# Kernel tuning notes

Hardware: AMD Instinct MI355X
Metric: run time of the kernel (lower is better)

Reference implementation:

```python
import jax, jax.numpy as jnp
import numpy as np

B, C, H, W = 32, 512, 32, 32
CI = C // 2  # inter_channels
EPS = 1e-5


def setup_inputs() -> dict:
    key = jax.random.key(0)
    ks = jax.random.split(key, 12)
    s = 0.02
    return {
        "x": jax.random.normal(ks[0], (B, C, H, W), jnp.float32),
        "w_g": jax.random.normal(ks[1], (CI, C), jnp.float32) * s,
        "b_g": jax.random.normal(ks[2], (CI,), jnp.float32) * s,
        "w_theta": jax.random.normal(ks[3], (CI, C), jnp.float32) * s,
        "b_theta": jax.random.normal(ks[4], (CI,), jnp.float32) * s,
        "w_phi": jax.random.normal(ks[5], (CI, C), jnp.float32) * s,
        "b_phi": jax.random.normal(ks[6], (CI,), jnp.float32) * s,
        "w_W": jax.random.normal(ks[7], (C, CI), jnp.float32) * s,
        "b_W": jax.random.normal(ks[8], (C,), jnp.float32) * s,
        "bn_gamma": jax.random.normal(ks[9], (C,), jnp.float32) * 0.1 + 1.0,
        "bn_beta": jax.random.normal(ks[10], (C,), jnp.float32) * 0.1,
        "bn_mean": jax.random.normal(ks[11], (C,), jnp.float32) * 0.1,
        "bn_var": jnp.abs(jax.random.normal(jax.random.fold_in(key, 99), (C,), jnp.float32)) * 0.5 + 0.5,
    }


def reference(x, w_g, b_g, w_theta, b_theta, w_phi, b_phi, w_W, b_W,
              bn_gamma, bn_beta, bn_mean, bn_var):
    b, c, h, w = x.shape
    n = h * w
    xf = x.reshape(b, c, n)  # [B, C, N]
    # 1x1 convs == per-pixel channel matmuls
    g = jnp.einsum('oc,bcn->bon', w_g, xf) + b_g[:, None]          # [B, Ci, N]
    theta = jnp.einsum('oc,bcn->bon', w_theta, xf) + b_theta[:, None]
    phi = jnp.einsum('oc,bcn->bon', w_phi, xf) + b_phi[:, None]
    # f[b, i, j] = theta_i . phi_j ; scaled by 1/N (softmax-free attention)
    f_div_C = jnp.einsum('bcn,bcm->bnm', theta, phi) / n           # [B, N, N]
    # y[b, c, n] = sum_m f[b, n, m] * g[b, c, m]
    y = jnp.einsum('bnm,bcm->bcn', f_div_C, g)                     # [B, Ci, N]
    # W: 1x1 conv back to C channels + BatchNorm (inference form)
    Wy = jnp.einsum('oi,bin->bon', w_W, y) + b_W[:, None]          # [B, C, N]
    inv_std = jax.lax.rsqrt(bn_var + EPS)
    bn = (Wy - bn_mean[:, None]) * (inv_std * bn_gamma)[:, None] + bn_beta[:, None]
    z = bn.reshape(b, c, h, w) + x
    return z
```

## Files before the change

kernel.cpp:

```cpp
#include <hip/hip_runtime.h>
#include <hip/hip_bf16.h>
#include <cstdint>
#include <cstddef>

using bf16 = __hip_bfloat16;
typedef __attribute__((ext_vector_type(8))) short short8v;
typedef __attribute__((ext_vector_type(4))) float f32x4;

static constexpr int BATCH = 32;
static constexpr int CH    = 512;
static constexpr int CIc   = 256;
static constexpr int NSP   = 1024;
#define EPSV 1e-5f

__device__ __forceinline__ bf16 f2bf(float f) { return __float2bfloat16(f); }

__device__ __forceinline__ void gload_lds16(const bf16* g, bf16* l) {
  __builtin_amdgcn_global_load_lds(
      (const __attribute__((address_space(1))) void*)g,
      (__attribute__((address_space(3))) void*)l, 16, 0, 0);
}

__global__ __launch_bounds__(256) void convert_weights(
    const float* __restrict__ wg, const float* __restrict__ wph, const float* __restrict__ wth,
    const float* __restrict__ bg, const float* __restrict__ bph, const float* __restrict__ bth,
    const float* __restrict__ wW,
    bf16* __restrict__ wcat, bf16* __restrict__ wWb, float* __restrict__ biascat)
{
  int i = blockIdx.x * 256 + threadIdx.x;
  const int WSZ = CIc * CH;
  if (i < WSZ) {
    wcat[i]         = f2bf(wg[i]);
    wcat[WSZ + i]   = f2bf(wph[i]);
    wcat[2*WSZ + i] = f2bf(wth[i]);
    wWb[i]          = f2bf(wW[i]);
  }
  if (i < CIc) {
    biascat[i]        = bg[i];
    biascat[CIc + i]  = bph[i];
    biascat[2*CIc + i]= bth[i];
  }
}

__global__ __launch_bounds__(256) void transpose_x_kernel(
    const float* __restrict__ x, bf16* __restrict__ xt)
{
  __shared__ bf16 t[32][34];
  int n0 = blockIdx.x * 32, c0 = blockIdx.y * 32, b = blockIdx.z;
  const float* s = x + (size_t)b * CH * NSP;
  bf16* d = xt + (size_t)b * NSP * CH;
  int tx = threadIdx.x & 31, ty = threadIdx.x >> 5;
  #pragma unroll
  for (int i = 0; i < 32; i += 8)
    t[ty + i][tx] = f2bf(s[(size_t)(c0 + ty + i) * NSP + n0 + tx]);
  __syncthreads();
  #pragma unroll
  for (int i = 0; i < 32; i += 8)
    d[(size_t)(n0 + ty + i) * CH + c0 + tx] = t[tx][ty + i];
}

template<int EPI>
__global__ __launch_bounds__(512, 4) void gemm_bt(
    const bf16* __restrict__ A, size_t sA,
    const bf16* __restrict__ Bm, size_t sB,
    void* __restrict__ Cm,
    int K,
    const float* __restrict__ bias,
    bf16* __restrict__ Tt,
    const float* __restrict__ bW, const float* __restrict__ gma,
    const float* __restrict__ bta, const float* __restrict__ mu,
    const float* __restrict__ var,
    const float* __restrict__ xres)
{
  __shared__ bf16 As[2][256 * 32];
  __shared__ bf16 Bs[2][128 * 32];
  int m0, n0, zb;
  if constexpr (EPI == 1) {
    int bidx = blockIdx.x;
    int wg = (bidx & 7) * 96 + (bidx >> 3);
    m0 = (wg >> 8) * 256;
    n0 = (wg & 255) * 128;
    zb = 0;
  } else {
    m0 = blockIdx.y * 256; n0 = blockIdx.x * 128; zb = blockIdx.z;
  }
  const bf16* Ab = A  + (size_t)zb * sA;
  const bf16* Bb = Bm + (size_t)zb * sB;
  const int tid  = threadIdx.x;
  const int wv   = tid >> 6, lane = tid & 63;
  const int l16  = lane & 15, g4 = lane >> 4;
  const int wr   = wv >> 1,  wc = wv & 1;

  f32x4 acc[4][4];
  #pragma unroll
  for (int i = 0; i < 4; ++i)
    #pragma unroll
    for (int j = 0; j < 4; ++j)
      acc[i][j] = (f32x4){0.f, 0.f, 0.f, 0.f};

  const int rq  = lane >> 2;
  const int oct = (lane & 3) ^ ((lane >> 3) & 3);
  auto stage = [&](int t, int p) {
    int kb = t * 32 + oct * 8;
    #pragma unroll
    for (int i = 0; i < 2; ++i) {
      int f = wv * 2 + i;
      gload_lds16(Ab + (size_t)(m0 + f * 16 + rq) * K + kb, &As[p][f * 512]);
    }
    gload_lds16(Bb + (size_t)(n0 + wv * 16 + rq) * K + kb, &Bs[p][wv * 512]);
  };

  const int rs = (g4 ^ ((l16 >> 1) & 3)) * 8;
  const int nt = K >> 5;
  stage(0, 0);
  __syncthreads();
  for (int t = 0; t < nt; ++t) {
    const int cur = t & 1;
    if (t + 1 < nt) stage(t + 1, cur ^ 1);
    short8v af[4], bfv[4];
    #pragma unroll
    for (int mf = 0; mf < 4; ++mf)
      af[mf] = *(const short8v*)&As[cur][(wr * 64 + mf * 16 + l16) * 32 + rs];
    #pragma unroll
    for (int nf = 0; nf < 4; ++nf)
      bfv[nf] = *(const short8v*)&Bs[cur][(wc * 64 + nf * 16 + l16) * 32 + rs];
    #pragma unroll
    for (int mf = 0; mf < 4; ++mf)
      #pragma unroll
      for (int nf = 0; nf < 4; ++nf)
        acc[mf][nf] = __builtin_amdgcn_mfma_f32_16x16x32_bf16(af[mf], bfv[nf], acc[mf][nf], 0, 0, 0);
    __syncthreads();
  }

  const int colbase = n0 + wc * 64 + l16;
  const int rowb    = wr * 64 + g4 * 4;

  if constexpr (EPI == 2) {
    #pragma unroll
    for (int mf = 0; mf < 4; ++mf) {
      #pragma unroll
      for (int j = 0; j < 4; ++j) {
        int row = m0 + rowb + mf * 16 + j;
        float a  = gma[row] * rsqrtf(var[row] + EPSV);
        float bb = (bW[row] - mu[row]) * a + bta[row];
        float sc = a * (1.f / (float)NSP);
        #pragma unroll
        for (int nf = 0; nf < 4; ++nf) {
          int col = colbase + nf * 16;
          size_t idx = (size_t)zb * (CH * NSP) + (size_t)row * NSP + col;
          ((float*)Cm)[idx] = acc[mf][nf][j] * sc + bb + ((const float*)xres)[idx];
        }
      }
    }
  } else {
    if (m0 < 512) {
      #pragma unroll
      for (int mf = 0; mf < 4; ++mf)
        #pragma unroll
        for (int j = 0; j < 4; ++j) {
          int row = m0 + rowb + mf * 16 + j;
          float badd = bias[row];
          #pragma unroll
          for (int nf = 0; nf < 4; ++nf) {
            int col = colbase + nf * 16;
            int b = col >> 10, n = col & 1023;
            ((bf16*)Cm)[(size_t)b * (CH * NSP) + (size_t)row * NSP + n] = f2bf(acc[mf][nf][j] + badd);
          }
        }
    } else {
      #pragma unroll
      for (int mf = 0; mf < 4; ++mf) {
        int ci0 = rowb + mf * 16;
        #pragma unroll
        for (int nf = 0; nf < 4; ++nf) {
          int col = colbase + nf * 16;
          int b = col >> 10, n = col & 1023;
          uint64_t pk = 0;
          #pragma unroll
          for (int j = 0; j < 4; ++j) {
            bf16 bv = f2bf(acc[mf][nf][j] + bias[512 + ci0 + j]);
            pk |= (uint64_t)(*(unsigned short*)&bv) << (16 * j);
          }
          *(uint64_t*)(Tt + (size_t)b * (NSP * CIc) + (size_t)n * CIc + ci0) = pk;
        }
      }
    }
  }
}

__global__ __launch_bounds__(256) void gemm_nt_small(
    const bf16* __restrict__ A, size_t sA,
    const bf16* __restrict__ Bm, size_t sB,
    bf16* __restrict__ Cm, size_t sC,
    int N, int K)
{
  __shared__ bf16 As[2][128 * 64];
  __shared__ bf16 Bs[2][128 * 64];
  const int b  = blockIdx.z;
  const int m0 = blockIdx.y * 128;
  const int n0 = blockIdx.x * 128;
  const bf16* Ab = A  + (size_t)b * sA;
  const bf16* Bb = Bm + (size_t)b * sB;
  const int tid  = threadIdx.x;
  const int wv   = tid >> 6, lane = tid & 63;
  const int l16  = lane & 15, g4 = lane >> 4;
  const int wr   = wv >> 1,  wc = wv & 1;

  f32x4 acc[4][4];
  #pragma unroll
  for (int i = 0; i < 4; ++i)
    #pragma unroll
    for (int j = 0; j < 4; ++j)
      acc[i][j] = (f32x4){0.f, 0.f, 0.f, 0.f};

  auto stage = [&](int ks, int p) {
    #pragma unroll
    for (int i = 0; i < 4; ++i) {
      int s = i * 256 + tid;
      int row = s >> 3, ch8 = (s & 7) << 3;
      gload_lds16(Ab + (size_t)(m0 + row) * K + ks + ch8, &As[p][(i * 256 + wv * 64) * 8]);
      gload_lds16(Bb + (size_t)(n0 + row) * K + ks + ch8, &Bs[p][(i * 256 + wv * 64) * 8]);
    }
  };

  const int nt = K >> 6;
  stage(0, 0);
  __syncthreads();
  for (int t = 0; t < nt; ++t) {
    const int cur = t & 1;
    if (t + 1 < nt) stage((t + 1) << 6, cur ^ 1);
    #pragma unroll
    for (int kk = 0; kk < 2; ++kk) {
      short8v af[4], bfv[4];
      #pragma unroll
      for (int mf = 0; mf < 4; ++mf)
        af[mf] = *(const short8v*)&As[cur][(wr * 64 + mf * 16 + l16) * 64 + kk * 32 + g4 * 8];
      #pragma unroll
      for (int nf = 0; nf < 4; ++nf)
        bfv[nf] = *(const short8v*)&Bs[cur][(wc * 64 + nf * 16 + l16) * 64 + kk * 32 + g4 * 8];
      #pragma unroll
      for (int mf = 0; mf < 4; ++mf)
        #pragma unroll
        for (int nf = 0; nf < 4; ++nf)
          acc[mf][nf] = __builtin_amdgcn_mfma_f32_16x16x32_bf16(af[mf], bfv[nf], acc[mf][nf], 0, 0, 0);
    }
    __syncthreads();
  }

  const int colbase = n0 + wc * 64 + l16;
  const int rowbase = m0 + wr * 64 + g4 * 4;
  #pragma unroll
  for (int mf = 0; mf < 4; ++mf)
    #pragma unroll
    for (int j = 0; j < 4; ++j) {
      int row = rowbase + mf * 16 + j;
      #pragma unroll
      for (int nf = 0; nf < 4; ++nf) {
        int col = colbase + nf * 16;
        Cm[(size_t)b * sC + (size_t)row * N + col] = f2bf(acc[mf][nf][j]);
      }
    }
}

extern "C" void kernel_launch(void* const* d_in, const int* in_sizes, int n_in,
                              void* d_out, int out_size, void* d_ws, size_t ws_size,
                              hipStream_t stream)
{
  const float* x    = (const float*)d_in[0];
  const float* w_g  = (const float*)d_in[1];
  const float* b_g  = (const float*)d_in[2];
  const float* w_th = (const float*)d_in[3];
  const float* b_th = (const float*)d_in[4];
  const float* w_ph = (const float*)d_in[5];
  const float* b_ph = (const float*)d_in[6];
  const float* w_W  = (const float*)d_in[7];
  const float* b_W  = (const float*)d_in[8];
  const float* gma  = (const float*)d_in[9];
  const float* bta  = (const float*)d_in[10];
  const float* mu   = (const float*)d_in[11];
  const float* var  = (const float*)d_in[12];
  float* out = (float*)d_out;

  char* ws = (char*)d_ws;
  bf16* proj = (bf16*)(ws + 0);
  bf16* xt   = (bf16*)(ws + 33554432);
  bf16* thT  = (bf16*)(ws + 67108864);
  bf16* S    = (bf16*)(ws + 83886080);
  bf16* T    = (bf16*)(ws + 88080384);
  bf16* wcat = (bf16*)(ws + 96468992);
  bf16* wWb  = (bf16*)(ws + 97255424);
  float* bcat= (float*)(ws + 97517568);

  convert_weights<<<512, 256, 0, stream>>>(w_g, w_ph, w_th, b_g, b_ph, b_th, w_W, wcat, wWb, bcat);
  transpose_x_kernel<<<dim3(32, 16, 32), 256, 0, stream>>>(x, xt);

  gemm_bt<1><<<dim3(768, 1, 1), 512, 0, stream>>>(
      wcat, 0, xt, 0, proj, CH, bcat, thT,
      nullptr, nullptr, nullptr, nullptr, nullptr, nullptr);

  gemm_nt_small<<<dim3(2, 2, 32), 256, 0, stream>>>(
      proj + 256 * 1024, (size_t)CH * NSP, proj, (size_t)CH * NSP, S, (size_t)CIc * CIc,
      CIc, NSP);

  gemm_nt_small<<<dim3(2, 4, 32), 256, 0, stream>>>(
      wWb, 0, S, (size_t)CIc * CIc, T, (size_t)CH * CIc,
      CIc, CIc);

  gemm_bt<2><<<dim3(8, 2, 32), 512, 0, stream>>>(
      T, (size_t)CH * CIc, thT, (size_t)NSP * CIc, out, CIc,
      nullptr, nullptr, b_W, gma, bta, mu, var, x);
}
```

Before: 132.1 us.

## Fuse x transpose and bf16 conversion into projection GEMM B-tile loading

Removes the separate transpose kernel and the xt bf16 workspace. The projection GEMM now reads fp32 x directly from global memory in its native [C,N] layout, converts each value to bf16 in registers, and writes swizzled B tiles into LDS, with the next tile's loads overlapped with the MFMA loop. This saves one kernel launch and a full write plus re-read of the transposed copy of x. In exchange, B loads become strided scalar fp32 reads issued through registers rather than direct global-to-LDS loads, which may lower load efficiency.

Measured after the change: 133.8 us. About the same (+1.3%).

```diff
diff --git a/kernel.cpp b/kernel.cpp
--- a/kernel.cpp
+++ b/kernel.cpp
@@ -42,31 +42,130 @@
   }
 }
 
-__global__ __launch_bounds__(256) void transpose_x_kernel(
-    const float* __restrict__ x, bf16* __restrict__ xt)
-{
-  __shared__ bf16 t[32][34];
-  int n0 = blockIdx.x * 32, c0 = blockIdx.y * 32, b = blockIdx.z;
-  const float* s = x + (size_t)b * CH * NSP;
-  bf16* d = xt + (size_t)b * NSP * CH;
-  int tx = threadIdx.x & 31, ty = threadIdx.x >> 5;
-  #pragma unroll
-  for (int i = 0; i < 32; i += 8)
-    t[ty + i][tx] = f2bf(s[(size_t)(c0 + ty + i) * NSP + n0 + tx]);
+__global__ __launch_bounds__(512, 4) void gemm_k1_fused(
+    const bf16* __restrict__ A,
+    const float* __restrict__ x,
+    bf16* __restrict__ Cm,
+    const float* __restrict__ bias,
+    bf16* __restrict__ Tt)
+{
+  constexpr int K = CH;
+  __shared__ bf16 As[2][256 * 32];
+  __shared__ bf16 Bs[2][128 * 32];
+  int bidx = blockIdx.x;
+  int wg = (bidx & 7) * 96 + (bidx >> 3);
+  const int m0 = (wg >> 8) * 256;
+  const int ncol = (wg & 255);
+  const int zb = ncol >> 3;
+  const int n0 = (ncol & 7) * 128;
+  const float* xb = x + (size_t)zb * (CH * NSP);
+  const int tid  = threadIdx.x;
+  const int wv   = tid >> 6, lane = tid & 63;
+  const int l16  = lane & 15, g4 = lane >> 4;
+  const int wr   = wv >> 1,  wc = wv & 1;
+
+  f32x4 acc[4][4];
+  #pragma unroll
+  for (int i = 0; i < 4; ++i)
+    #pragma unroll
+    for (int j = 0; j < 4; ++j)
+      acc[i][j] = (f32x4){0.f, 0.f, 0.f, 0.f};
+
+  const int rq  = lane >> 2;
+  const int aoct = (lane & 3) ^ ((lane >> 3) & 3);
+  auto stageA = [&](int t, int p) {
+    int kb = t * 32 + aoct * 8;
+    #pragma unroll
+    for (int i = 0; i < 2; ++i) {
+      int f = wv * 2 + i;
+      gload_lds16(A + (size_t)(m0 + f * 16 + rq) * K + kb, &As[p][f * 512]);
+    }
+  };
+
+  const int colq = tid >> 2;
+  const int octq = tid & 3;
+  const int bslot = octq ^ ((colq >> 1) & 3);
+  float vb[8];
+  auto loadB = [&](int t) {
+    const float* xp = xb + (size_t)(t * 32 + octq * 8) * NSP + n0 + colq;
+    #pragma unroll
+    for (int i = 0; i < 8; ++i) vb[i] = xp[(size_t)i * NSP];
+  };
+  auto writeB = [&](int p) {
+    short8v pk;
+    #pragma unroll
+    for (int i = 0; i < 8; ++i) {
+      bf16 bv = f2bf(vb[i]);
+      pk[i] = *(short*)&bv;
+    }
+    *(short8v*)&Bs[p][colq * 32 + bslot * 8] = pk;
+  };
+
+  const int rs = (g4 ^ ((l16 >> 1) & 3)) * 8;
+  const int nt = K >> 5;
+  loadB(0); stageA(0, 0); writeB(0);
   __syncthreads();
-  #pragma unroll
-  for (int i = 0; i < 32; i += 8)
-    d[(size_t)(n0 + ty + i) * CH + c0 + tx] = t[tx][ty + i];
-}
-
-template<int EPI>
-__global__ __launch_bounds__(512, 4) void gemm_bt(
+  for (int t = 0; t < nt; ++t) {
+    const int cur = t & 1;
+    if (t + 1 < nt) { stageA(t + 1, cur ^ 1); loadB(t + 1); }
+    short8v af[4], bfv[4];
+    #pragma unroll
+    for (int mf = 0; mf < 4; ++mf)
+      af[mf] = *(const short8v*)&As[cur][(wr * 64 + mf * 16 + l16) * 32 + rs];
+    #pragma unroll
+    for (int nf = 0; nf < 4; ++nf)
+      bfv[nf] = *(const short8v*)&Bs[cur][(wc * 64 + nf * 16 + l16) * 32 + rs];
+    #pragma unroll
+    for (int mf = 0; mf < 4; ++mf)
+      #pragma unroll
+      for (int nf = 0; nf < 4; ++nf)
+        acc[mf][nf] = __builtin_amdgcn_mfma_f32_16x16x32_bf16(af[mf], bfv[nf], acc[mf][nf], 0, 0, 0);
+    if (t + 1 < nt) writeB(cur ^ 1);
+    __syncthreads();
+  }
+
+  const int colbase = n0 + (zb << 10) + wc * 64 + l16;
+  const int rowb    = wr * 64 + g4 * 4;
+
+  if (m0 < 512) {
+    #pragma unroll
+    for (int mf = 0; mf < 4; ++mf)
+      #pragma unroll
+      for (int j = 0; j < 4; ++j) {
+        int row = m0 + rowb + mf * 16 + j;
+        float badd = bias[row];
+        #pragma unroll
+        for (int nf = 0; nf < 4; ++nf) {
+          int col = colbase + nf * 16;
+          int b = col >> 10, n = col & 1023;
+          Cm[(size_t)b * (CH * NSP) + (size_t)row * NSP + n] = f2bf(acc[mf][nf][j] + badd);
+        }
+      }
+  } else {
+    #pragma unroll
+    for (int mf = 0; mf < 4; ++mf) {
+      int ci0 = rowb + mf * 16;
+      #pragma unroll
+      for (int nf = 0; nf < 4; ++nf) {
+        int col = colbase + nf * 16;
+        int b = col >> 10, n = col & 1023;
+        uint64_t pk = 0;
+        #pragma unroll
+        for (int j = 0; j < 4; ++j) {
+          bf16 bv = f2bf(acc[mf][nf][j] + bias[512 + ci0 + j]);
+          pk |= (uint64_t)(*(unsigned short*)&bv) << (16 * j);
+        }
+        *(uint64_t*)(Tt + (size_t)b * (NSP * CIc) + (size_t)n * CIc + ci0) = pk;
+      }
+    }
+  }
+}
+
+__global__ __launch_bounds__(512, 4) void gemm_bt2(
     const bf16* __restrict__ A, size_t sA,
     const bf16* __restrict__ Bm, size_t sB,
-    void* __restrict__ Cm,
+    float* __restrict__ Cm,
     int K,
-    const float* __restrict__ bias,
-    bf16* __restrict__ Tt,
     const float* __restrict__ bW, const float* __restrict__ gma,
     const float* __restrict__ bta, const float* __restrict__ mu,
     const float* __restrict__ var,
@@ -74,16 +173,7 @@
 {
   __shared__ bf16 As[2][256 * 32];
   __shared__ bf16 Bs[2][128 * 32];
-  int m0, n0, zb;
-  if constexpr (EPI == 1) {
-    int bidx = blockIdx.x;
-    int wg = (bidx & 7) * 96 + (bidx >> 3);
-    m0 = (wg >> 8) * 256;
-    n0 = (wg & 255) * 128;
-    zb = 0;
-  } else {
-    m0 = blockIdx.y * 256; n0 = blockIdx.x * 128; zb = blockIdx.z;
-  }
+  const int m0 = blockIdx.y * 256, n0 = blockIdx.x * 128, zb = blockIdx.z;
   const bf16* Ab = A  + (size_t)zb * sA;
   const bf16* Bb = Bm + (size_t)zb * sB;
   const int tid  = threadIdx.x;
@@ -134,55 +224,19 @@
 
   const int colbase = n0 + wc * 64 + l16;
   const int rowb    = wr * 64 + g4 * 4;
-
-  if constexpr (EPI == 2) {
-    #pragma unroll
-    for (int mf = 0; mf < 4; ++mf) {
-      #pragma unroll
-      for (int j = 0; j < 4; ++j) {
-        int row = m0 + rowb + mf * 16 + j;
-        float a  = gma[row] * rsqrtf(var[row] + EPSV);
-        float bb = (bW[row] - mu[row]) * a + bta[row];
-        float sc = a * (1.f / (float)NSP);
-        #pragma unroll
-        for (int nf = 0; nf < 4; ++nf) {
-          int col = colbase + nf * 16;
-          size_t idx = (size_t)zb * (CH * NSP) + (size_t)row * NSP + col;
-          ((float*)Cm)[idx] = acc[mf][nf][j] * sc + bb + ((const float*)xres)[idx];
-        }
-      }
-    }
-  } else {
-    if (m0 < 512) {
-      #pragma unroll
-      for (int mf = 0; mf < 4; ++mf)
-        #pragma unroll
-        for (int j = 0; j < 4; ++j) {
-          int row = m0 + rowb + mf * 16 + j;
-          float badd = bias[row];
-          #pragma unroll
-          for (int nf = 0; nf < 4; ++nf) {
-            int col = colbase + nf * 16;
-            int b = col >> 10, n = col & 1023;
-            ((bf16*)Cm)[(size_t)b * (CH * NSP) + (size_t)row * NSP + n] = f2bf(acc[mf][nf][j] + badd);
-          }
-        }
-    } else {
-      #pragma unroll
-      for (int mf = 0; mf < 4; ++mf) {
-        int ci0 = rowb + mf * 16;
-        #pragma unroll
-        for (int nf = 0; nf < 4; ++nf) {
-          int col = colbase + nf * 16;
-          int b = col >> 10, n = col & 1023;
-          uint64_t pk = 0;
-          #pragma unroll
-          for (int j = 0; j < 4; ++j) {
-            bf16 bv = f2bf(acc[mf][nf][j] + bias[512 + ci0 + j]);
-            pk |= (uint64_t)(*(unsigned short*)&bv) << (16 * j);
-          }
-          *(uint64_t*)(Tt + (size_t)b * (NSP * CIc) + (size_t)n * CIc + ci0) = pk;
-        }
+  #pragma unroll
+  for (int mf = 0; mf < 4; ++mf) {
+    #pragma unroll
+    for (int j = 0; j < 4; ++j) {
+      int row = m0 + rowb + mf * 16 + j;
+      float a  = gma[row] * rsqrtf(var[row] + EPSV);
+      float bb = (bW[row] - mu[row]) * a + bta[row];
+      float sc = a * (1.f / (float)NSP);
+      #pragma unroll
+      for (int nf = 0; nf < 4; ++nf) {
+        int col = colbase + nf * 16;
+        size_t idx = (size_t)zb * (CH * NSP) + (size_t)row * NSP + col;
+        Cm[idx] = acc[mf][nf][j] * sc + bb + xres[idx];
       }
     }
   }
@@ -283,7 +337,6 @@
 
   char* ws = (char*)d_ws;
   bf16* proj = (bf16*)(ws + 0);
-  bf16* xt   = (bf16*)(ws + 33554432);
   bf16* thT  = (bf16*)(ws + 67108864);
   bf16* S    = (bf16*)(ws + 83886080);
   bf16* T    = (bf16*)(ws + 88080384);
@@ -292,11 +345,8 @@
   float* bcat= (float*)(ws + 97517568);
 
   convert_weights<<<512, 256, 0, stream>>>(w_g, w_ph, w_th, b_g, b_ph, b_th, w_W, wcat, wWb, bcat);
-  transpose_x_kernel<<<dim3(32, 16, 32), 256, 0, stream>>>(x, xt);
-
-  gemm_bt<1><<<dim3(768, 1, 1), 512, 0, stream>>>(
-      wcat, 0, xt, 0, proj, CH, bcat, thT,
-      nullptr, nullptr, nullptr, nullptr, nullptr, nullptr);
+
+  gemm_k1_fused<<<dim3(768, 1, 1), 512, 0, stream>>>(wcat, x, proj, bcat, thT);
 
   gemm_nt_small<<<dim3(2, 2, 32), 256, 0, stream>>>(
       proj + 256 * 1024, (size_t)CH * NSP, proj, (size_t)CH * NSP, S, (size_t)CIc * CIc,
@@ -306,7 +356,7 @@
       wWb, 0, S, (size_t)CIc * CIc, T, (size_t)CH * CIc,
       CIc, CIc);
 
-  gemm_bt<2><<<dim3(8, 2, 32), 512, 0, stream>>>(
+  gemm_bt2<<<dim3(8, 2, 32), 512, 0, stream>>>(
       T, (size_t)CH * CIc, thT, (size_t)NSP * CIc, out, CIc,
-      nullptr, nullptr, b_W, gma, bta, mu, var, x);
-}
+      b_W, gma, bta, mu, var, x);
+}
```
